# Optimization experiments

Measured on AMD Instinct MI355X. Metric: run time of the kernel, lower is better.

## Reference

```python
import jax, jax.numpy as jnp
import numpy as np

GRID_SIZE = 5
SPLINE_ORDER = 3
IN_F, OUT_F = 1024, 1024
N_BASIS = GRID_SIZE + 1 + 2 * SPLINE_ORDER  # 12 knots (matches basis last dim)


def _make_grid():
    g = jnp.linspace(-1.0, 1.0, GRID_SIZE + 1)
    return jnp.concatenate([jnp.full((SPLINE_ORDER,), g[0]), g, jnp.full((SPLINE_ORDER,), g[-1])])


def setup_inputs() -> dict:
    key = jax.random.key(0)
    k1, k2, k3 = jax.random.split(key, 3)
    x = jax.random.normal(k1, (4, 2048, IN_F), dtype=jnp.float32)
    spline_weight = jax.random.normal(k2, (OUT_F, IN_F, N_BASIS), dtype=jnp.float32) * 0.1
    base_weight = jax.random.normal(k3, (OUT_F, IN_F), dtype=jnp.float32) * 0.1
    return {"x": x, "spline_weight": spline_weight, "base_weight": base_weight}


def reference(x, spline_weight, base_weight):
    grid = _make_grid()  # (N_BASIS,)
    # base linear: F.linear(x, W) = x @ W.T
    base_out = jnp.einsum('bsi,oi->bso', x, base_weight)
    # tent-shaped basis: relu(1 - |(x - knot) * grid_size / 2|), shape (b,s,in,N_BASIS)
    xc = jnp.clip(x, -1.0, 1.0)
    basis = jax.nn.relu(1.0 - jnp.abs((xc[..., None] - grid) * (GRID_SIZE / 2.0)))
    spline_out = jnp.einsum('bsik,oik->bso', basis, spline_weight)
    return base_out + spline_out
```

## Files before the change

### kernel.cpp

```cpp
#include <hip/hip_runtime.h>


#define IN_F   1024
#define OUT_F  1024
#define M_DIM  8192
#define N_DIM  1024
#define KP     9
#define K_DIM  (IN_F * KP)
#define BK     128
#define NTILES (K_DIM / BK)

typedef __attribute__((ext_vector_type(4)))  int   i32x4;
typedef __attribute__((ext_vector_type(4)))  float f32x4;
typedef __attribute__((ext_vector_type(16))) char  char16v;

#define SX   (6.0f / 127.0f)
#define ISX  (127.0f / 6.0f)
#define ISL  (16129.0f / 3.0f)
#define TB   (0.7f / 127.0f)
#define ITB  (127.0f / 0.7f)
#define ITL  (16129.0f / 0.35f)
#define ITE  (127.0f / 1.4f)

__device__ __constant__ float SCALES[9] = {
    4.2f / 16129.0f,
    2.1f / 2048383.0f,
    2.1f / 2048383.0f,
    1.4f / 16129.0f,
    0.7f / 16129.0f,
    0.7f / 16129.0f,
    0.7f / 16129.0f,
    0.7f / 16129.0f,
    1.4f / 16129.0f
};

__device__ inline float clampf(float v, float lo, float hi) {
    return fminf(fmaxf(v, lo), hi);
}

__global__ void expand_q(const float* __restrict__ x, signed char* __restrict__ Aq) {
    int idx = blockIdx.x * 256 + threadIdx.x;
    int m = idx >> 6, i16 = idx & 63;
    const float4* xp = reinterpret_cast<const float4*>(x + ((size_t)m << 10) + i16 * 16);
    float v[16];
    #pragma unroll
    for (int q = 0; q < 4; ++q) {
        float4 f = xp[q];
        v[4*q] = f.x; v[4*q+1] = f.y; v[4*q+2] = f.z; v[4*q+3] = f.w;
    }
    signed char out[9][16];
    #pragma unroll
    for (int e = 0; e < 16; ++e) {
        float xe = v[e];
        float xh = clampf(rintf(xe * ISX), -127.f, 127.f);
        float xl = xe - xh * SX;
        out[0][e] = (signed char)(int)xh;
        out[1][e] = (signed char)(int)xh;
        out[2][e] = (signed char)(int)clampf(rintf(xl * ISL), -127.f, 127.f);
        float xc = clampf(xe, -1.f, 1.f);
        #pragma unroll
        for (int j = 0; j < 6; ++j) {
            float t = -1.f + 0.4f * (float)j;
            float h = fmaxf(1.f - fabsf((xc - t) * 2.5f), 0.f);
            out[3 + j][e] = (signed char)(int)rintf(h * 127.f);
        }
    }
    size_t base = (size_t)m * K_DIM + i16 * 16;
    #pragma unroll
    for (int p = 0; p < 9; ++p) {
        char16v pk;
        #pragma unroll
        for (int e = 0; e < 16; ++e) pk[e] = out[p][e];
        *reinterpret_cast<char16v*>(Aq + base + (size_t)p * 1024) = pk;
    }
}

__global__ void fold_q(const float* __restrict__ sw, const float* __restrict__ bw,
                       signed char* __restrict__ Bq) {
    int idx = blockIdx.x * 256 + threadIdx.x;
    int o = idx >> 8, i4 = idx & 255;
    signed char out[9][4];
    #pragma unroll
    for (int e = 0; e < 4; ++e) {
        int i = i4 * 4 + e;
        const float4* p = reinterpret_cast<const float4*>(sw + (size_t)(o * 1024 + i) * 12);
        float4 a = p[0];
        float4 b = p[1];
        float4 c = p[2];
        float w = bw[o * 1024 + i];
        float wh = clampf(rintf(w * ITB), -127.f, 127.f);
        float wl = w - wh * TB;
        out[0][e] = (signed char)(int)wh;
        out[1][e] = (signed char)(int)clampf(rintf(wl * ITL), -127.f, 127.f);
        out[2][e] = (signed char)(int)wh;
        out[3][e] = (signed char)(int)clampf(rintf((a.x + a.y + a.z + a.w) * ITE), -127.f, 127.f);
        out[4][e] = (signed char)(int)clampf(rintf(b.x * ITB), -127.f, 127.f);
        out[5][e] = (signed char)(int)clampf(rintf(b.y * ITB), -127.f, 127.f);
        out[6][e] = (signed char)(int)clampf(rintf(b.z * ITB), -127.f, 127.f);
        out[7][e] = (signed char)(int)clampf(rintf(b.w * ITB), -127.f, 127.f);
        out[8][e] = (signed char)(int)clampf(rintf((c.x + c.y + c.z + c.w) * ITE), -127.f, 127.f);
    }
    size_t base = (size_t)o * K_DIM + i4 * 4;
    #pragma unroll
    for (int p = 0; p < 9; ++p) {
        char4 pk;
        pk.x = out[p][0]; pk.y = out[p][1]; pk.z = out[p][2]; pk.w = out[p][3];
        *reinterpret_cast<char4*>(Bq + base + (size_t)p * 1024) = pk;
    }
}

__global__ __launch_bounds__(256, 2) void gemm_q(
        const signed char* __restrict__ Aq,
        const signed char* __restrict__ Bq,
        float* __restrict__ C) {
    __shared__ signed char As[2][128 * BK];
    __shared__ signed char Bs[2][128 * BK];

    const int tid  = threadIdx.x;
    const int wave = tid >> 6;
    const int lane = tid & 63;
    const int wr   = wave >> 1;
    const int wc   = wave & 1;

    const int orig = blockIdx.x;
    const int wg   = (orig & 7) * 64 + (orig >> 3);
    const int bx   = wg & 7;
    const int by   = wg >> 3;

    const int srow  = tid >> 3;
    const int scolb = ((tid & 7) * 16) ^ ((srow & 7) << 4);

#define STAGE(BUF, T) do {                                                      \
    int kt_ = ((T) < NTILES ? (T) : NTILES - 1) * BK;                           \
    _Pragma("unroll")                                                           \
    for (int u = 0; u < 4; ++u) {                                               \
        const signed char* ga_ = Aq + (size_t)(by * 128 + u * 32 + srow) * K_DIM + kt_ + scolb; \
        const signed char* gb_ = Bq + (size_t)(bx * 128 + u * 32 + srow) * K_DIM + kt_ + scolb; \
        __builtin_amdgcn_global_load_lds(                                       \
            (const __attribute__((address_space(1))) void*)ga_,                 \
            (__attribute__((address_space(3))) void*)(As[BUF] + u * 4096 + wave * 1024), 16, 0, 0); \
        __builtin_amdgcn_global_load_lds(                                       \
            (const __attribute__((address_space(1))) void*)gb_,                 \
            (__attribute__((address_space(3))) void*)(Bs[BUF] + u * 4096 + wave * 1024), 16, 0, 0); \
    }                                                                           \
} while (0)

    i32x4 acci[4][4];
    f32x4 accf[4][4];
    #pragma unroll
    for (int m2 = 0; m2 < 4; ++m2)
        #pragma unroll
        for (int n2 = 0; n2 < 4; ++n2) {
            acci[m2][n2] = (i32x4){0, 0, 0, 0};
            accf[m2][n2] = (f32x4){0.f, 0.f, 0.f, 0.f};
        }

    STAGE(0, 0);

    for (int t = 0; t < NTILES; ++t) {
        const int cur = t & 1;
        __syncthreads();
        STAGE(cur ^ 1, t + 1);

        i32x4 af[8], bf[8];
        #pragma unroll
        for (int m2 = 0; m2 < 4; ++m2)
            #pragma unroll
            for (int kk = 0; kk < 2; ++kk) {
                int row = wr * 64 + m2 * 16 + (lane & 15);
                int off = row * BK + ((kk * 64 + (lane >> 4) * 16) ^ ((row & 7) << 4));
                af[m2 * 2 + kk] = *reinterpret_cast<const i32x4*>(&As[cur][off]);
            }
        #pragma unroll
        for (int n2 = 0; n2 < 4; ++n2)
            #pragma unroll
            for (int kk = 0; kk < 2; ++kk) {
                int row = wc * 64 + n2 * 16 + (lane & 15);
                int off = row * BK + ((kk * 64 + (lane >> 4) * 16) ^ ((row & 7) << 4));
                bf[n2 * 2 + kk] = *reinterpret_cast<const i32x4*>(&Bs[cur][off]);
            }

        __builtin_amdgcn_s_setprio(1);
        #pragma unroll
        for (int m2 = 0; m2 < 4; ++m2)
            #pragma unroll
            for (int n2 = 0; n2 < 4; ++n2)
                #pragma unroll
                for (int kk = 0; kk < 2; ++kk)
                    acci[m2][n2] = __builtin_amdgcn_mfma_i32_16x16x64_i8(
                        af[m2 * 2 + kk], bf[n2 * 2 + kk], acci[m2][n2], 0, 0, 0);
        __builtin_amdgcn_s_setprio(0);

        if ((t & 7) == 7) {
            float s = SCALES[t >> 3];
            #pragma unroll
            for (int m2 = 0; m2 < 4; ++m2)
                #pragma unroll
                for (int n2 = 0; n2 < 4; ++n2) {
                    #pragma unroll
                    for (int r = 0; r < 4; ++r)
                        accf[m2][n2][r] += s * (float)acci[m2][n2][r];
                    acci[m2][n2] = (i32x4){0, 0, 0, 0};
                }
        }
    }

    #pragma unroll
    for (int m2 = 0; m2 < 4; ++m2)
        #pragma unroll
        for (int n2 = 0; n2 < 4; ++n2) {
            const int row = by * 128 + wr * 64 + m2 * 16 + ((lane >> 4) << 2);
            const int col = bx * 128 + wc * 64 + n2 * 16 + (lane & 15);
            #pragma unroll
            for (int r = 0; r < 4; ++r)
                C[(size_t)(row + r) * N_DIM + col] = accf[m2][n2][r];
        }
#undef STAGE
}

extern "C" void kernel_launch(void* const* d_in, const int* in_sizes, int n_in,
                              void* d_out, int out_size, void* d_ws, size_t ws_size,
                              hipStream_t stream) {
    const float* x  = (const float*)d_in[0];
    const float* sw = (const float*)d_in[1];
    const float* bw = (const float*)d_in[2];
    float* out = (float*)d_out;

    signed char* Aq = (signed char*)d_ws;
    signed char* Bq = (signed char*)d_ws + (size_t)M_DIM * K_DIM;

    expand_q<<<(M_DIM * 64) / 256, 256, 0, stream>>>(x, Aq);
    fold_q<<<(OUT_F * 256) / 256, 256, 0, stream>>>(sw, bw, Bq);
    gemm_q<<<(M_DIM / 128) * (N_DIM / 128), 256, 0, stream>>>(Aq, Bq, out);
}
```

Baseline: 114.5 us.

## Pre-pack B in MFMA fragment order and load it directly from global

The weight-folding kernel now writes the quantized B matrix in a layout that matches the per-lane MFMA fragment order. The GEMM reads B fragments straight from global memory into registers instead of staging them through LDS, which halves shared-memory use and the LDS traffic per tile. The change also drops the block-index swizzle and reorders the MFMA loop so kk is outermost. The trade-off is that B loads are no longer shared across waves through LDS and are not prefetched, so their global/L2 latency lands on the critical path each iteration and L2 locality may get worse.

New measurement: 134.8 us. +17.7%, slower.

```diff
diff --git a/kernel.cpp b/kernel.cpp
--- a/kernel.cpp
+++ b/kernel.cpp
@@ -9,6 +9,7 @@
 #define K_DIM  (IN_F * KP)
 #define BK     128
 #define NTILES (K_DIM / BK)
+#define NKT    (K_DIM / 64)
 
 typedef __attribute__((ext_vector_type(4)))  int   i32x4;
 typedef __attribute__((ext_vector_type(4)))  float f32x4;
@@ -76,7 +77,7 @@
 }
 
 __global__ void fold_q(const float* __restrict__ sw, const float* __restrict__ bw,
-                       signed char* __restrict__ Bq) {
+                       signed char* __restrict__ Bp) {
     int idx = blockIdx.x * 256 + threadIdx.x;
     int o = idx >> 8, i4 = idx & 255;
     signed char out[9][4];
@@ -100,21 +101,23 @@
         out[7][e] = (signed char)(int)clampf(rintf(b.w * ITB), -127.f, 127.f);
         out[8][e] = (signed char)(int)clampf(rintf((c.x + c.y + c.z + c.w) * ITE), -127.f, 127.f);
     }
-    size_t base = (size_t)o * K_DIM + i4 * 4;
+    const int g      = o >> 4;
+    const int lane   = (o & 15) + 16 * ((i4 >> 2) & 3);
+    const int byteof = (i4 & 3) * 4;
     #pragma unroll
     for (int p = 0; p < 9; ++p) {
+        int kt = p * 16 + (i4 >> 4);
         char4 pk;
         pk.x = out[p][0]; pk.y = out[p][1]; pk.z = out[p][2]; pk.w = out[p][3];
-        *reinterpret_cast<char4*>(Bq + base + (size_t)p * 1024) = pk;
+        *reinterpret_cast<char4*>(Bp + (((size_t)g * NKT + kt) * 64 + lane) * 16 + byteof) = pk;
     }
 }
 
 __global__ __launch_bounds__(256, 2) void gemm_q(
         const signed char* __restrict__ Aq,
-        const signed char* __restrict__ Bq,
+        const signed char* __restrict__ Bp,
         float* __restrict__ C) {
-    __shared__ signed char As[2][128 * BK];
-    __shared__ signed char Bs[2][128 * BK];
+    __shared__ __align__(16) signed char As[2][128 * BK];
 
     const int tid  = threadIdx.x;
     const int wave = tid >> 6;
@@ -122,10 +125,8 @@
     const int wr   = wave >> 1;
     const int wc   = wave & 1;
 
-    const int orig = blockIdx.x;
-    const int wg   = (orig & 7) * 64 + (orig >> 3);
-    const int bx   = wg & 7;
-    const int by   = wg >> 3;
+    const int bx   = blockIdx.x & 7;
+    const int by   = blockIdx.x >> 3;
 
     const int srow  = tid >> 3;
     const int scolb = ((tid & 7) * 16) ^ ((srow & 7) << 4);
@@ -135,13 +136,9 @@
     _Pragma("unroll")                                                           \
     for (int u = 0; u < 4; ++u) {                                               \
         const signed char* ga_ = Aq + (size_t)(by * 128 + u * 32 + srow) * K_DIM + kt_ + scolb; \
-        const signed char* gb_ = Bq + (size_t)(bx * 128 + u * 32 + srow) * K_DIM + kt_ + scolb; \
         __builtin_amdgcn_global_load_lds(                                       \
             (const __attribute__((address_space(1))) void*)ga_,                 \
             (__attribute__((address_space(3))) void*)(As[BUF] + u * 4096 + wave * 1024), 16, 0, 0); \
-        __builtin_amdgcn_global_load_lds(                                       \
-            (const __attribute__((address_space(1))) void*)gb_,                 \
-            (__attribute__((address_space(3))) void*)(Bs[BUF] + u * 4096 + wave * 1024), 16, 0, 0); \
     }                                                                           \
 } while (0)
 
@@ -154,6 +151,8 @@
             acci[m2][n2] = (i32x4){0, 0, 0, 0};
             accf[m2][n2] = (f32x4){0.f, 0.f, 0.f, 0.f};
         }
+
+    const size_t bwv = ((size_t)(bx * 8 + wc * 4) * NKT) * 1024 + (size_t)lane * 16;
 
     STAGE(0, 0);
 
@@ -162,7 +161,15 @@
         __syncthreads();
         STAGE(cur ^ 1, t + 1);
 
-        i32x4 af[8], bf[8];
+        i32x4 bf[8];
+        #pragma unroll
+        for (int n2 = 0; n2 < 4; ++n2)
+            #pragma unroll
+            for (int kk = 0; kk < 2; ++kk)
+                bf[n2 * 2 + kk] = *reinterpret_cast<const i32x4*>(
+                    Bp + bwv + ((size_t)n2 * NKT + 2 * t + kk) * 1024);
+
+        i32x4 af[8];
         #pragma unroll
         for (int m2 = 0; m2 < 4; ++m2)
             #pragma unroll
@@ -171,22 +178,14 @@
                 int off = row * BK + ((kk * 64 + (lane >> 4) * 16) ^ ((row & 7) << 4));
                 af[m2 * 2 + kk] = *reinterpret_cast<const i32x4*>(&As[cur][off]);
             }
-        #pragma unroll
-        for (int n2 = 0; n2 < 4; ++n2)
-            #pragma unroll
-            for (int kk = 0; kk < 2; ++kk) {
-                int row = wc * 64 + n2 * 16 + (lane & 15);
-                int off = row * BK + ((kk * 64 + (lane >> 4) * 16) ^ ((row & 7) << 4));
-                bf[n2 * 2 + kk] = *reinterpret_cast<const i32x4*>(&Bs[cur][off]);
-            }
 
         __builtin_amdgcn_s_setprio(1);
         #pragma unroll
-        for (int m2 = 0; m2 < 4; ++m2)
-            #pragma unroll
-            for (int n2 = 0; n2 < 4; ++n2)
+        for (int kk = 0; kk < 2; ++kk)
+            #pragma unroll
+            for (int m2 = 0; m2 < 4; ++m2)
                 #pragma unroll
-                for (int kk = 0; kk < 2; ++kk)
+                for (int n2 = 0; n2 < 4; ++n2)
                     acci[m2][n2] = __builtin_amdgcn_mfma_i32_16x16x64_i8(
                         af[m2 * 2 + kk], bf[n2 * 2 + kk], acci[m2][n2], 0, 0, 0);
         __builtin_amdgcn_s_setprio(0);
@@ -227,9 +226,9 @@
     float* out = (float*)d_out;
 
     signed char* Aq = (signed char*)d_ws;
-    signed char* Bq = (signed char*)d_ws + (size_t)M_DIM * K_DIM;
+    signed char* Bp = (signed char*)d_ws + (size_t)M_DIM * K_DIM;
 
     expand_q<<<(M_DIM * 64) / 256, 256, 0, stream>>>(x, Aq);
-    fold_q<<<(OUT_F * 256) / 256, 256, 0, stream>>>(sw, bw, Bq);
-    gemm_q<<<(M_DIM / 128) * (N_DIM / 128), 256, 0, stream>>>(Aq, Bq, out);
-}
+    fold_q<<<(OUT_F * 256) / 256, 256, 0, stream>>>(sw, bw, Bp);
+    gemm_q<<<(M_DIM / 128) * (N_DIM / 128), 256, 0, stream>>>(Aq, Bp, out);
+}
```
